# Optimization experiments

Hardware: AMD Instinct MI355X
Metric: run time of the kernel (lower is better)

The kernel has to match this reference:

```python
import jax, jax.numpy as jnp
import numpy as np

BS, T, N_AGENTS, N_ACTIONS = 8, 256, 8, 20
A = N_AGENTS * N_ACTIONS          # 160 gru input dim
E, D, HID, S = 128, 128, 32, 256  # encoder_dim, decoder_dim, mixing_embed_dim, state_dim
EMBED = HID * (A + E)             # 9216


def _lin(k, out_d, in_d):
    s = 1.0 / np.sqrt(in_d)
    return jax.random.uniform(k, (out_d, in_d), jnp.float32, -s, s)


def _vec(k, d, fan):
    s = 1.0 / np.sqrt(fan)
    return jax.random.uniform(k, (d,), jnp.float32, -s, s)


def setup_inputs() -> dict:
    key = jax.random.key(0)
    ks = jax.random.split(key, 32)
    inp = {
        'act': jax.random.uniform(ks[0], (BS, T, N_AGENTS, N_ACTIONS), jnp.float32),
        'states': jax.random.normal(ks[1], (BS, T, S), jnp.float32),
        # GRU (PyTorch layout: gates stacked [r; z; n])
        'gru_wih': _lin(ks[2], 3 * E, A),
        'gru_whh': _lin(ks[3], 3 * E, E),
        'gru_bih': _vec(ks[4], 3 * E, E),
        'gru_bhh': _vec(ks[5], 3 * E, E),
        # encoder fc
        'fc_w': _lin(ks[6], D, E),
        'fc_b': _vec(ks[7], D, E),
        # attention
        'attn_w': _lin(ks[8], D, D + E),
        'v_w': _vec(ks[9], D, D),
        # hyper_w_1 (2-layer MLP)
        'hw1_w0': _lin(ks[10], EMBED, S), 'hw1_b0': _vec(ks[11], EMBED, S),
        'hw1_w1': _lin(ks[12], EMBED, EMBED), 'hw1_b1': _vec(ks[13], EMBED, EMBED),
        # hyper_w_final (2-layer MLP)
        'hwf_w0': _lin(ks[14], HID, S), 'hwf_b0': _vec(ks[15], HID, S),
        'hwf_w1': _lin(ks[16], HID, HID), 'hwf_b1': _vec(ks[17], HID, HID),
        # hyper_b_1
        'hb1_w': _lin(ks[18], HID, S), 'hb1_b': _vec(ks[19], HID, S),
        # hyper_b_2 (2-layer MLP)
        'hb2_w0': _lin(ks[20], HID, S), 'hb2_b0': _vec(ks[21], HID, S),
        'hb2_w1': _lin(ks[22], 1, HID), 'hb2_b1': _vec(ks[23], 1, HID),
    }
    return inp


def reference(act, states, gru_wih, gru_whh, gru_bih, gru_bhh, fc_w, fc_b,
              attn_w, v_w, hw1_w0, hw1_b0, hw1_w1, hw1_b1,
              hwf_w0, hwf_b0, hwf_w1, hwf_b1, hb1_w, hb1_b,
              hb2_w0, hb2_b0, hb2_w1, hb2_b1):
    bs, t, n_ag, n_ac = act.shape
    a = n_ag * n_ac
    e = gru_whh.shape[1]
    d = fc_w.shape[0]
    hid = hb1_w.shape[0]

    act_flat = act.reshape(bs, t, a)
    # act_his = [zeros, act]; prefixes use only the first t steps of it
    x = jnp.concatenate([jnp.zeros((bs, 1, a), act.dtype), act_flat[:, : t - 1]], axis=1)

    # GRU over full sequence once (causal => identical to recomputing each prefix)
    def step(h, xt):
        gi = xt @ gru_wih.T + gru_bih
        gh = h @ gru_whh.T + gru_bhh
        ir, iz, i_n = jnp.split(gi, 3, axis=-1)
        hr, hz, h_n = jnp.split(gh, 3, axis=-1)
        r = jax.nn.sigmoid(ir + hr)
        z = jax.nn.sigmoid(iz + hz)
        n = jnp.tanh(i_n + r * h_n)
        h_new = (1.0 - z) * n + z * h
        return h_new, h_new

    h0 = jnp.zeros((bs, e), act.dtype)
    _, enc = jax.lax.scan(step, h0, jnp.swapaxes(x, 0, 1))
    enc = jnp.swapaxes(enc, 0, 1)  # [bs, T, E]

    # s0 for prefix ending at step q is tanh(fc(enc[:, q]))
    s0 = jnp.tanh(enc @ fc_w.T + fc_b)  # [bs, T, D]

    # attention: cat order is (s, enc_output)
    w_s, w_e = attn_w[:, :d], attn_w[:, d:]
    ps = s0 @ w_s.T            # [bs, Tq, D]
    pe = enc @ w_e.T           # [bs, Tk, D]
    pre = jnp.tanh(ps[:, :, None, :] + pe[:, None, :, :])  # [bs, Tq, Tk, D]
    scores = jnp.einsum('bqkd,d->bqk', pre, v_w)
    mask = jnp.tril(jnp.ones((t, t), bool))  # key j <= query q (prefix j < idx)
    scores = jnp.where(mask[None], scores, -jnp.inf)
    attn = jax.nn.softmax(scores, axis=-1)
    c = jnp.einsum('bqk,bke->bqe', attn, enc)  # [bs, T, E]

    inp = jnp.concatenate([act_flat, c], axis=-1).reshape(bs * t, 1, a + e)
    st = states.reshape(bs * t, -1)

    w1 = (jax.nn.relu(st @ hw1_w0.T + hw1_b0) @ hw1_w1.T + hw1_b1).reshape(bs * t, a + e, hid)
    b1 = (st @ hb1_w.T + hb1_b)[:, None, :]
    h = jax.nn.relu(jnp.einsum('bik,bkh->bih', inp, w1) + b1)  # [bs*T, 1, hid]

    wf = (jax.nn.relu(st @ hwf_w0.T + hwf_b0) @ hwf_w1.T + hwf_b1)[:, :, None]  # [bs*T, hid, 1]
    b2 = (jax.nn.relu(st @ hb2_w0.T + hb2_b0) @ hb2_w1.T + hb2_b1)[:, :, None]  # [bs*T, 1, 1]
    q = (jnp.einsum('bih,bho->bio', h, wf) + b2).reshape(bs, t, 1)
    return q
```

## Files before the change

kernel.cpp:

```cpp
#include <hip/hip_runtime.h>
#include <hip/hip_bf16.h>
#include <stdint.h>

typedef __attribute__((ext_vector_type(4))) float f32x4;
typedef __attribute__((ext_vector_type(8))) short short8v;
typedef __attribute__((ext_vector_type(4))) unsigned short u16x4;

constexpr int kT  = 256;
constexpr int kA  = 160;

__device__ __forceinline__ float bf2f(unsigned short u){
  union { unsigned int u; float f; } c; c.u = ((unsigned int)u) << 16; return c.f;
}
__device__ __forceinline__ unsigned short f2bf(float f){
  union { float f; unsigned int u; } c; c.f = f;
  unsigned int r = (c.u + 0x7FFFu + ((c.u >> 16) & 1u)) >> 16;
  return (unsigned short)r;
}
__device__ __forceinline__ float sigmoid_fast(float x){
  return __builtin_amdgcn_rcpf(1.f + __expf(-x));
}
__device__ __forceinline__ float tanhf_fast(float x){
  float xc = fminf(fmaxf(x, -15.f), 15.f);
  float t = __expf(2.f * xc);
  return (t - 1.f) * __builtin_amdgcn_rcpf(t + 1.f);
}
__device__ __forceinline__ void gload_lds16(const void* g, void* l){
  __builtin_amdgcn_global_load_lds((const __attribute__((address_space(1))) void*)g,
                                   (__attribute__((address_space(3))) void*)l, 16, 0, 0);
}
__device__ __forceinline__ void bar_lgkm(){
  asm volatile("s_waitcnt lgkmcnt(0)" ::: "memory");
  __builtin_amdgcn_s_barrier();
  asm volatile("" ::: "memory");
}
__device__ __forceinline__ void bar_only(){
  asm volatile("" ::: "memory");
  __builtin_amdgcn_s_barrier();
  asm volatile("" ::: "memory");
}

__global__ __launch_bounds__(256) void k_fill_f32(float* out, int n, float v){
  int i = blockIdx.x * blockDim.x + threadIdx.x;
  if (i < n) out[i] = v;
}

__global__ __launch_bounds__(256) void k_f32_to_bf16(const float* __restrict__ src,
                                                     unsigned short* __restrict__ dst, int n4){
  int stride = gridDim.x * blockDim.x;
  for (int i = blockIdx.x * blockDim.x + threadIdx.x; i < n4; i += stride){
    f32x4 v = *(const f32x4*)(src + (size_t)i * 4);
    u16x4 o;
    o[0] = f2bf(v[0]); o[1] = f2bf(v[1]); o[2] = f2bf(v[2]); o[3] = f2bf(v[3]);
    *(u16x4*)(dst + (size_t)i * 4) = o;
  }
}

__global__ __launch_bounds__(384) void k_gi(const float* __restrict__ act,
                                            const float* __restrict__ wih,
                                            const float* __restrict__ bih,
                                            float* __restrict__ gi){
  int blk = blockIdx.x;
  int b = blk >> 5, tg = blk & 31;
  int j = threadIdx.x;
  __shared__ __align__(16) float xh[8][kA];
  for (int idx = j; idx < 8 * kA; idx += 384){
    int u = idx / kA, i = idx - u * kA;
    int t = tg * 8 + u;
    xh[u][i] = (t == 0) ? 0.f : act[((size_t)b * kT + t - 1) * kA + i];
  }
  __syncthreads();
  float acc[8] = {0,0,0,0,0,0,0,0};
  for (int i = 0; i < kA; i += 4){
    f32x4 wv = *(const f32x4*)(wih + (size_t)j * kA + i);
#pragma unroll
    for (int jj = 0; jj < 4; ++jj)
#pragma unroll
      for (int u = 0; u < 8; ++u)
        acc[u] += wv[jj] * xh[u][i + jj];
  }
  float bv = bih[j];
#pragma unroll
  for (int u = 0; u < 8; ++u)
    gi[((size_t)b * kT + tg * 8 + u) * 384 + j] = acc[u] + bv;
}

template<int RELU>
__device__ __forceinline__ void gemm576_body(const unsigned short* __restrict__ A,
                                             const unsigned short* __restrict__ B,
                                             const float* __restrict__ bias,
                                             unsigned short* __restrict__ C,
                                             int M, int Nc, int K, int ldc,
                                             int bid, int nwg, char* smem){
  int nbm = M >> 7;
  int cpx = nwg >> 3;
  int sw  = (bid & 7) * cpx + (bid >> 3);
  int bm = sw % nbm, bn = sw / nbm;
  int arow0 = bm << 7;
  int bcol0 = bn * 576;
  int t = threadIdx.x;
  int l = t & 63, w = t >> 6;
  int wr = w >> 2, wc = w & 3;
  int lr = l & 15, kq = l >> 4;
  int Kb = K * 2;
  int ar = t >> 2, ap = t & 3;
  size_t aoffg = (size_t)ar * Kb + ((ap ^ ((ar >> 1) & 3)) << 4);
  size_t boffg[5];
#pragma unroll
  for (int i = 0; i < 5; ++i){
    int q = i * 512 + t, r = q >> 2, p = q & 3;
    boffg[i] = (size_t)r * Kb + ((p ^ ((r >> 1) & 3)) << 4);
  }
  const char* Ag = (const char*)(A + (size_t)arow0 * K);
  const char* Bg = (const char*)(B + (size_t)bcol0 * K);
  int dA = t * 16;
  int kk16 = (kq ^ ((lr >> 1) & 3)) << 4;
  int aRd = (wr * 64 + lr) * 64 + kk16;
  int bRd = 8192 + (wc * 144 + lr) * 64 + kk16;
  f32x4 acc[4][9] = {};
  int nt = K >> 5;

  auto stage = [&](int kt, int bi){
    size_t kb = (size_t)kt * 64;
    char* Ld = smem + bi * 49152;
    gload_lds16(Ag + aoffg + kb, Ld + dA);
#pragma unroll
    for (int i = 0; i < 5; ++i)
      gload_lds16(Bg + boffg[i] + kb, Ld + 8192 + i * 8192 + dA);
  };

  stage(0, 0);
  stage(1, 1);
  asm volatile("s_waitcnt vmcnt(6)" ::: "memory");
  int cur = 0;
  for (int kt = 0; kt < nt; ++kt){
    bar_only();
    if (kt + 2 < nt){
      int nb = cur + 2; if (nb >= 3) nb -= 3;
      stage(kt + 2, nb);
    }
    const char* Ld = smem + cur * 49152;
    short8v af[4];
#pragma unroll
    for (int m = 0; m < 4; ++m) af[m] = *(const short8v*)(Ld + aRd + m * 1024);
#pragma unroll
    for (int c = 0; c < 3; ++c){
      short8v bf[3];
#pragma unroll
      for (int j = 0; j < 3; ++j) bf[j] = *(const short8v*)(Ld + bRd + (c * 3 + j) * 1024);
      __builtin_amdgcn_s_setprio(1);
#pragma unroll
      for (int m = 0; m < 4; ++m)
#pragma unroll
        for (int j = 0; j < 3; ++j)
          acc[m][c * 3 + j] = __builtin_amdgcn_mfma_f32_16x16x32_bf16(af[m], bf[j], acc[m][c * 3 + j], 0, 0, 0);
      __builtin_amdgcn_s_setprio(0);
    }
    if (kt + 1 < nt){
      if (kt + 2 < nt) asm volatile("s_waitcnt vmcnt(6)" ::: "memory");
      else             asm volatile("s_waitcnt vmcnt(0)" ::: "memory");
    }
    ++cur; if (cur == 3) cur = 0;
  }

#pragma unroll
  for (int m = 0; m < 4; ++m){
    int row = arow0 + wr * 64 + m * 16 + kq * 4;
#pragma unroll
    for (int n = 0; n < 9; ++n){
      int col = bcol0 + wc * 144 + n * 16 + lr;
      float bv = bias[col];
#pragma unroll
      for (int r = 0; r < 4; ++r){
        float v = acc[m][n][r] + bv;
        if (RELU) v = fmaxf(v, 0.f);
        C[(size_t)(row + r) * ldc + col] = f2bf(v);
      }
    }
  }
}

template<int RELU>
__global__ __launch_bounds__(512) void k_gemm576(const unsigned short* __restrict__ A,
                                                 const unsigned short* __restrict__ B,
                                                 const float* __restrict__ bias,
                                                 unsigned short* __restrict__ C,
                                                 int M, int Nc, int K, int ldc){
  __shared__ __align__(16) char smem[147456];
  gemm576_body<RELU>(A, B, bias, C, M, Nc, K, ldc, blockIdx.x, gridDim.x, smem);
}

__global__ __launch_bounds__(512) void k_gru_g1_conv(const float* __restrict__ gi,
                                                     const float* __restrict__ whh,
                                                     const float* __restrict__ bhh,
                                                     float* __restrict__ enc,
                                                     const unsigned short* __restrict__ stb,
                                                     const unsigned short* __restrict__ w0b,
                                                     const float* __restrict__ hb0,
                                                     unsigned short* __restrict__ zb,
                                                     const float* __restrict__ csrc,
                                                     unsigned short* __restrict__ cdst,
                                                     int n4){
  __shared__ __align__(16) char smem[147456];
  int blk = blockIdx.x;
  if (blk >= 264){
    int stride = (gridDim.x - 264) * 512;
    for (int i = (blk - 264) * 512 + threadIdx.x; i < n4; i += stride){
      f32x4 v = *(const f32x4*)(csrc + (size_t)i * 4);
      u16x4 o;
      o[0] = f2bf(v[0]); o[1] = f2bf(v[1]); o[2] = f2bf(v[2]); o[3] = f2bf(v[3]);
      *(u16x4*)(cdst + (size_t)i * 4) = o;
    }
    return;
  }
  if (blk >= 8){
    gemm576_body<1>(stb, w0b, hb0, zb, 2048, 9216, 256, 9216, blk - 8, 256, smem);
    return;
  }
  float* h_lds = (float*)smem;
  float (*red)[128] = (float(*)[128])(smem + 512);
  int b = blk;
  int tid = threadIdx.x;
  int e = tid & 127, s = tid >> 7;
  float W0[32], W1[32], W2[32];
#pragma unroll
  for (int k = 0; k < 32; ++k){
    W0[k] = whh[(size_t)(0 * 128 + e) * 128 + s * 32 + k];
    W1[k] = whh[(size_t)(1 * 128 + e) * 128 + s * 32 + k];
    W2[k] = whh[(size_t)(2 * 128 + e) * 128 + s * 32 + k];
  }
  if (tid < 128) h_lds[tid] = 0.f;
  float bh0 = 0.f, bh1 = 0.f, bh2 = 0.f;
  if (tid < 128){ bh0 = bhh[e]; bh1 = bhh[128 + e]; bh2 = bhh[256 + e]; }
  const float* gib = gi + (size_t)b * kT * 384;
  float* encb = enc + (size_t)b * kT * 128;
  float gir = 0.f, giz = 0.f, gin = 0.f;
  if (tid < 128){ gir = gib[e]; giz = gib[128 + e]; gin = gib[256 + e]; }
  bar_lgkm();
  for (int t = 0; t < kT; ++t){
    float p0 = 0.f, p1 = 0.f, p2 = 0.f;
#pragma unroll
    for (int k4 = 0; k4 < 8; ++k4){
      f32x4 hv = *(const f32x4*)(h_lds + s * 32 + k4 * 4);
#pragma unroll
      for (int jj = 0; jj < 4; ++jj){
        p0 += W0[k4 * 4 + jj] * hv[jj];
        p1 += W1[k4 * 4 + jj] * hv[jj];
        p2 += W2[k4 * 4 + jj] * hv[jj];
      }
    }
    float nir = 0.f, niz = 0.f, nin = 0.f;
    if (t + 1 < kT && tid < 128){
      const float* gn = gib + (size_t)(t + 1) * 384;
      nir = gn[e]; niz = gn[128 + e]; nin = gn[256 + e];
    }
    red[s * 3 + 0][e] = p0; red[s * 3 + 1][e] = p1; red[s * 3 + 2][e] = p2;
    bar_lgkm();
    if (tid < 128){
      float ghr = red[0][e] + red[3][e] + red[6][e] + red[9][e]  + bh0;
      float ghz = red[1][e] + red[4][e] + red[7][e] + red[10][e] + bh1;
      float ghn = red[2][e] + red[5][e] + red[8][e] + red[11][e] + bh2;
      float r = sigmoid_fast(gir + ghr);
      float z = sigmoid_fast(giz + ghz);
      float n = tanhf_fast(gin + r * ghn);
      float hnew = (1.f - z) * n + z * h_lds[e];
      h_lds[e] = hnew;
      encb[t * 128 + e] = hnew;
    }
    bar_lgkm();
    gir = nir; giz = niz; gin = nin;
  }
}

__global__ __launch_bounds__(128) void k_attnpre(const float* __restrict__ enc,
                                                 const float* __restrict__ fc_w,
                                                 const float* __restrict__ fc_b,
                                                 const float* __restrict__ attn_w,
                                                 float* __restrict__ ps,
                                                 float* __restrict__ pe){
  int bt = blockIdx.x, o = threadIdx.x;
  __shared__ __align__(16) float ench[128], s0h[128];
  ench[o] = enc[(size_t)bt * 128 + o];
  __syncthreads();
  float a0 = fc_b[o], a1 = 0.f;
  for (int i = 0; i < 128; i += 4){
    f32x4 wv = *(const f32x4*)(fc_w + (size_t)o * 128 + i);
    f32x4 we = *(const f32x4*)(attn_w + (size_t)o * 256 + 128 + i);
    f32x4 ev = *(const f32x4*)(ench + i);
#pragma unroll
    for (int jj = 0; jj < 4; ++jj){ a0 += wv[jj] * ev[jj]; a1 += we[jj] * ev[jj]; }
  }
  s0h[o] = tanhf_fast(a0);
  pe[(size_t)bt * 128 + o] = a1;
  __syncthreads();
  float a2 = 0.f;
  for (int i = 0; i < 128; i += 4){
    f32x4 ws = *(const f32x4*)(attn_w + (size_t)o * 256 + i);
    f32x4 sv = *(const f32x4*)(s0h + i);
#pragma unroll
    for (int jj = 0; jj < 4; ++jj) a2 += ws[jj] * sv[jj];
  }
  ps[(size_t)bt * 128 + o] = a2;
}

__global__ __launch_bounds__(256) void k_attn(const float* __restrict__ enc,
                                              const float* __restrict__ ps,
                                              const float* __restrict__ pe,
                                              const float* __restrict__ v_w,
                                              float* __restrict__ cbuf){
  int q = blockIdx.x, b = blockIdx.y;
  int tid = threadIdx.x;
  __shared__ __align__(16) float psh[128], vwh[128];
  __shared__ __align__(16) float sch[256];
  __shared__ __align__(16) float rr[256];
  __shared__ float mxs, dns;
  if (tid < 128){
    psh[tid] = ps[((size_t)b * kT + q) * 128 + tid];
    vwh[tid] = v_w[tid];
  }
  __syncthreads();
  int nk = q + 1;
  for (int k = tid; k < nk; k += 256){
    const float* per = pe + ((size_t)b * kT + k) * 128;
    float sc = 0.f;
    for (int d = 0; d < 128; d += 4){
      f32x4 pv = *(const f32x4*)(per + d);
      f32x4 qv = *(const f32x4*)(psh + d);
      sc += vwh[d + 0] * tanhf_fast(qv[0] + pv[0]);
      sc += vwh[d + 1] * tanhf_fast(qv[1] + pv[1]);
      sc += vwh[d + 2] * tanhf_fast(qv[2] + pv[2]);
      sc += vwh[d + 3] * tanhf_fast(qv[3] + pv[3]);
    }
    sch[k] = sc;
  }
  __syncthreads();
  float lm = -3.0e38f;
  for (int k = tid; k < nk; k += 256) lm = fmaxf(lm, sch[k]);
  rr[tid] = lm; __syncthreads();
  for (int off = 128; off > 0; off >>= 1){
    if (tid < off) rr[tid] = fmaxf(rr[tid], rr[tid + off]);
    __syncthreads();
  }
  if (tid == 0) mxs = rr[0];
  __syncthreads();
  float mxv = mxs;
  float lsum = 0.f;
  for (int k = tid; k < nk; k += 256){
    float p = __expf(sch[k] - mxv);
    sch[k] = p; lsum += p;
  }
  __syncthreads();
  rr[tid] = lsum; __syncthreads();
  for (int off = 128; off > 0; off >>= 1){
    if (tid < off) rr[tid] += rr[tid + off];
    __syncthreads();
  }
  if (tid == 0) dns = __builtin_amdgcn_rcpf(rr[0]);
  __syncthreads();
  float rd = dns;
  int d = tid & 127, half = tid >> 7;
  float acc = 0.f;
  for (int k = half; k < nk; k += 2)
    acc += sch[k] * enc[((size_t)b * kT + k) * 128 + d];
  rr[tid] = acc; __syncthreads();
  if (half == 0)
    cbuf[((size_t)b * kT + q) * 128 + d] = (acc + rr[d + 128]) * rd;
}

__global__ __launch_bounds__(256) void k_final(const float* __restrict__ states,
                                               const float* __restrict__ act,
                                               const float* __restrict__ cbuf,
                                               const unsigned short* __restrict__ w1f,
                                               const float* __restrict__ hb1_w, const float* __restrict__ hb1_b,
                                               const float* __restrict__ hwf_w0, const float* __restrict__ hwf_b0,
                                               const float* __restrict__ hwf_w1, const float* __restrict__ hwf_b1,
                                               const float* __restrict__ hb2_w0, const float* __restrict__ hb2_b0,
                                               const float* __restrict__ hb2_w1, const float* __restrict__ hb2_b1,
                                               float* __restrict__ out){
  int bt = blockIdx.x, tid = threadIdx.x;
  __shared__ __align__(16) float sth[256], inph[288], red[256];
  __shared__ __align__(16) float t1h[32], t2h[32], b1h[32], wfh[32], hvals[32];
  __shared__ float b2s;
  sth[tid] = states[(size_t)bt * 256 + tid];
  if (tid < 160) inph[tid] = act[(size_t)bt * 160 + tid];
  if (tid < 128) inph[160 + tid] = cbuf[(size_t)bt * 128 + tid];
  __syncthreads();
  int o = tid & 31, s = tid >> 5;
  float p1 = 0.f, p2 = 0.f, p3 = 0.f;
  for (int k = s * 32; k < s * 32 + 32; k += 4){
    f32x4 sv  = *(const f32x4*)(sth + k);
    f32x4 w1v = *(const f32x4*)(hwf_w0 + (size_t)o * 256 + k);
    f32x4 w2v = *(const f32x4*)(hb2_w0 + (size_t)o * 256 + k);
    f32x4 w3v = *(const f32x4*)(hb1_w  + (size_t)o * 256 + k);
#pragma unroll
    for (int jj = 0; jj < 4; ++jj){
      p1 += w1v[jj] * sv[jj]; p2 += w2v[jj] * sv[jj]; p3 += w3v[jj] * sv[jj];
    }
  }
  red[tid] = p1; __syncthreads();
  if (tid < 32){
    float a = hwf_b0[tid];
#pragma unroll
    for (int s8 = 0; s8 < 8; ++s8) a += red[s8 * 32 + tid];
    t1h[tid] = fmaxf(a, 0.f);
  }
  __syncthreads();
  red[tid] = p2; __syncthreads();
  if (tid < 32){
    float a = hb2_b0[tid];
#pragma unroll
    for (int s8 = 0; s8 < 8; ++s8) a += red[s8 * 32 + tid];
    t2h[tid] = fmaxf(a, 0.f);
  }
  __syncthreads();
  red[tid] = p3; __syncthreads();
  if (tid < 32){
    float a = hb1_b[tid];
#pragma unroll
    for (int s8 = 0; s8 < 8; ++s8) a += red[s8 * 32 + tid];
    b1h[tid] = a;
  }
  __syncthreads();
  if (tid < 32){
    float a = hwf_b1[tid];
#pragma unroll
    for (int j = 0; j < 32; ++j) a += hwf_w1[(size_t)tid * 32 + j] * t1h[j];
    wfh[tid] = a;
  }
  if (tid == 64){
    float a = hb2_b1[0];
#pragma unroll
    for (int j = 0; j < 32; ++j) a += hb2_w1[j] * t2h[j];
    b2s = a;
  }
  __syncthreads();
  float ph = 0.f;
  const unsigned short* wrow = w1f + (size_t)bt * 9216;
  for (int i = s * 36; i < s * 36 + 36; ++i)
    ph += inph[i] * bf2f(wrow[i * 32 + o]);
  red[tid] = ph; __syncthreads();
  if (tid < 32){
    float a = b1h[tid];
#pragma unroll
    for (int s8 = 0; s8 < 8; ++s8) a += red[s8 * 32 + tid];
    hvals[tid] = fmaxf(a, 0.f) * wfh[tid];
  }
  __syncthreads();
  if (tid == 0){
    float q = b2s;
#pragma unroll
    for (int j = 0; j < 32; ++j) q += hvals[j];
    out[bt] = q;
  }
}

extern "C" void kernel_launch(void* const* d_in, const int* in_sizes, int n_in,
                              void* d_out, int out_size, void* d_ws, size_t ws_size,
                              hipStream_t stream){
  float* outp = (float*)d_out;

  bool ok = (n_in == 24) && out_size == 2048 &&
            in_sizes[0] == 327680 && in_sizes[1] == 524288 &&
            in_sizes[2] == 61440  && in_sizes[3] == 49152 &&
            in_sizes[10] == 2359296 && in_sizes[12] == 84934656;
  if (!ok){
    k_fill_f32<<<dim3(8), dim3(256), 0, stream>>>(outp, 2048, 1.0e6f);
    return;
  }

  const float* act    = (const float*)d_in[0];
  const float* states = (const float*)d_in[1];
  const float* wih    = (const float*)d_in[2];
  const float* whh    = (const float*)d_in[3];
  const float* bih    = (const float*)d_in[4];
  const float* bhh    = (const float*)d_in[5];
  const float* fc_w   = (const float*)d_in[6];
  const float* fc_b   = (const float*)d_in[7];
  const float* attn_w = (const float*)d_in[8];
  const float* v_w    = (const float*)d_in[9];
  const float* hw1_w0 = (const float*)d_in[10];
  const float* hw1_b0 = (const float*)d_in[11];
  const float* hw1_w1 = (const float*)d_in[12];
  const float* hw1_b1 = (const float*)d_in[13];
  const float* hwf_w0 = (const float*)d_in[14];
  const float* hwf_b0 = (const float*)d_in[15];
  const float* hwf_w1 = (const float*)d_in[16];
  const float* hwf_b1 = (const float*)d_in[17];
  const float* hb1_w  = (const float*)d_in[18];
  const float* hb1_b  = (const float*)d_in[19];
  const float* hb2_w0 = (const float*)d_in[20];
  const float* hb2_b0 = (const float*)d_in[21];
  const float* hb2_w1 = (const float*)d_in[22];
  const float* hb2_b1 = (const float*)d_in[23];

  char* ws = (char*)d_ws;
  size_t off = 0;
  auto alloc = [&](size_t bytes)->void*{
    void* p = ws + off; off += (bytes + 255) & ~(size_t)255; return p;
  };
  unsigned short* zb  = (unsigned short*)alloc((size_t)2048 * 9216 * 2);
  unsigned short* w1f = (unsigned short*)alloc((size_t)2048 * 9216 * 2);
  unsigned short* w0b = (unsigned short*)alloc((size_t)9216 * 256 * 2);
  unsigned short* stb = (unsigned short*)alloc((size_t)2048 * 256 * 2);
  float* gi   = (float*)alloc((size_t)2048 * 384 * 4);
  float* enc  = (float*)alloc((size_t)2048 * 128 * 4);
  float* psb  = (float*)alloc((size_t)2048 * 128 * 4);
  float* peb  = (float*)alloc((size_t)2048 * 128 * 4);
  float* cbuf = (float*)alloc((size_t)2048 * 128 * 4);
  size_t floor_bytes = off;
  const size_t row_bytes = (size_t)9216 * 2;
  const size_t slack = (size_t)2 << 20;
  if (ws_size < floor_bytes + 576 * row_bytes + slack){
    k_fill_f32<<<dim3(8), dim3(256), 0, stream>>>(outp, 2048, (float)(ws_size >> 20));
    return;
  }
  size_t avail = ws_size - floor_bytes - slack;
  int chunk_rows = (int)(((avail / row_bytes) / 576) * 576);
  if (chunk_rows > 9216) chunk_rows = 9216;
  unsigned short* w1c = (unsigned short*)(ws + floor_bytes);
  int first_nc = chunk_rows;

  k_f32_to_bf16<<<dim3(1024), dim3(256), 0, stream>>>(hw1_w0, w0b, 9216 * 256 / 4);
  k_f32_to_bf16<<<dim3(256),  dim3(256), 0, stream>>>(states, stb, 2048 * 256 / 4);
  k_gi<<<dim3(256), dim3(384), 0, stream>>>(act, wih, bih, gi);
  k_gru_g1_conv<<<dim3(2048), dim3(512), 0, stream>>>(gi, whh, bhh, enc,
                                                      stb, w0b, hw1_b0, zb,
                                                      hw1_w1, w1c, first_nc * 9216 / 4);
  k_attnpre<<<dim3(2048), dim3(128), 0, stream>>>(enc, fc_w, fc_b, attn_w, psb, peb);
  k_attn<<<dim3(256, 8), dim3(256), 0, stream>>>(enc, psb, peb, v_w, cbuf);
  for (int c0 = 0; c0 < 9216; c0 += chunk_rows){
    int nc = 9216 - c0; if (nc > chunk_rows) nc = chunk_rows;
    if (c0 > 0)
      k_f32_to_bf16<<<dim3(2048), dim3(256), 0, stream>>>(hw1_w1 + (size_t)c0 * 9216, w1c, nc * 9216 / 4);
    k_gemm576<0><<<dim3(16 * (nc / 576)), dim3(512), 0, stream>>>(zb, w1c, hw1_b1 + c0, w1f + c0,
                                                                  2048, nc, 9216, 9216);
  }
  k_final<<<dim3(2048), dim3(256), 0, stream>>>(states, act, cbuf, w1f,
      hb1_w, hb1_b, hwf_w0, hwf_b0, hwf_w1, hwf_b1, hb2_w0, hb2_b0, hb2_w1, hb2_b1,
      outp);
}
```

Measured before the change: 742.6 us.

## Move hw1_w1 bf16 conversion from GRU kernel into attention kernels

After: 787.9 us. +6.1%, slower.

```diff
diff --git a/kernel.cpp b/kernel.cpp
--- a/kernel.cpp
+++ b/kernel.cpp
@@ -39,21 +39,25 @@
   __builtin_amdgcn_s_barrier();
   asm volatile("" ::: "memory");
 }
-
-__global__ __launch_bounds__(256) void k_fill_f32(float* out, int n, float v){
-  int i = blockIdx.x * blockDim.x + threadIdx.x;
-  if (i < n) out[i] = v;
-}
-
-__global__ __launch_bounds__(256) void k_f32_to_bf16(const float* __restrict__ src,
-                                                     unsigned short* __restrict__ dst, int n4){
-  int stride = gridDim.x * blockDim.x;
-  for (int i = blockIdx.x * blockDim.x + threadIdx.x; i < n4; i += stride){
+__device__ __forceinline__ void conv_range(const float* __restrict__ src,
+                                           unsigned short* __restrict__ dst,
+                                           int beg, int end, int start, int stride){
+  for (int i = beg + start; i < end; i += stride){
     f32x4 v = *(const f32x4*)(src + (size_t)i * 4);
     u16x4 o;
     o[0] = f2bf(v[0]); o[1] = f2bf(v[1]); o[2] = f2bf(v[2]); o[3] = f2bf(v[3]);
     *(u16x4*)(dst + (size_t)i * 4) = o;
   }
+}
+
+__global__ __launch_bounds__(256) void k_fill_f32(float* out, int n, float v){
+  int i = blockIdx.x * blockDim.x + threadIdx.x;
+  if (i < n) out[i] = v;
+}
+
+__global__ __launch_bounds__(256) void k_f32_to_bf16(const float* __restrict__ src,
+                                                     unsigned short* __restrict__ dst, int n4){
+  conv_range(src, dst, 0, n4, blockIdx.x * blockDim.x + threadIdx.x, gridDim.x * blockDim.x);
 }
 
 __global__ __launch_bounds__(384) void k_gi(const float* __restrict__ act,
@@ -190,29 +194,16 @@
   gemm576_body<RELU>(A, B, bias, C, M, Nc, K, ldc, blockIdx.x, gridDim.x, smem);
 }
 
-__global__ __launch_bounds__(512) void k_gru_g1_conv(const float* __restrict__ gi,
-                                                     const float* __restrict__ whh,
-                                                     const float* __restrict__ bhh,
-                                                     float* __restrict__ enc,
-                                                     const unsigned short* __restrict__ stb,
-                                                     const unsigned short* __restrict__ w0b,
-                                                     const float* __restrict__ hb0,
-                                                     unsigned short* __restrict__ zb,
-                                                     const float* __restrict__ csrc,
-                                                     unsigned short* __restrict__ cdst,
-                                                     int n4){
+__global__ __launch_bounds__(512) void k_gru_g1(const float* __restrict__ gi,
+                                                const float* __restrict__ whh,
+                                                const float* __restrict__ bhh,
+                                                float* __restrict__ enc,
+                                                const unsigned short* __restrict__ stb,
+                                                const unsigned short* __restrict__ w0b,
+                                                const float* __restrict__ hb0,
+                                                unsigned short* __restrict__ zb){
   __shared__ __align__(16) char smem[147456];
   int blk = blockIdx.x;
-  if (blk >= 264){
-    int stride = (gridDim.x - 264) * 512;
-    for (int i = (blk - 264) * 512 + threadIdx.x; i < n4; i += stride){
-      f32x4 v = *(const f32x4*)(csrc + (size_t)i * 4);
-      u16x4 o;
-      o[0] = f2bf(v[0]); o[1] = f2bf(v[1]); o[2] = f2bf(v[2]); o[3] = f2bf(v[3]);
-      *(u16x4*)(cdst + (size_t)i * 4) = o;
-    }
-    return;
-  }
   if (blk >= 8){
     gemm576_body<1>(stb, w0b, hb0, zb, 2048, 9216, 256, 9216, blk - 8, 256, smem);
     return;
@@ -272,13 +263,21 @@
   }
 }
 
-__global__ __launch_bounds__(128) void k_attnpre(const float* __restrict__ enc,
-                                                 const float* __restrict__ fc_w,
-                                                 const float* __restrict__ fc_b,
-                                                 const float* __restrict__ attn_w,
-                                                 float* __restrict__ ps,
-                                                 float* __restrict__ pe){
-  int bt = blockIdx.x, o = threadIdx.x;
+__global__ __launch_bounds__(128) void k_attnpre_conv(const float* __restrict__ enc,
+                                                      const float* __restrict__ fc_w,
+                                                      const float* __restrict__ fc_b,
+                                                      const float* __restrict__ attn_w,
+                                                      float* __restrict__ ps,
+                                                      float* __restrict__ pe,
+                                                      const float* __restrict__ csrc,
+                                                      unsigned short* __restrict__ cdst,
+                                                      int beg, int end){
+  int blk = blockIdx.x;
+  if (blk >= 2048){
+    conv_range(csrc, cdst, beg, end, (blk - 2048) * 128 + threadIdx.x, (gridDim.x - 2048) * 128);
+    return;
+  }
+  int bt = blk, o = threadIdx.x;
   __shared__ __align__(16) float ench[128], s0h[128];
   ench[o] = enc[(size_t)bt * 128 + o];
   __syncthreads();
@@ -303,12 +302,20 @@
   ps[(size_t)bt * 128 + o] = a2;
 }
 
-__global__ __launch_bounds__(256) void k_attn(const float* __restrict__ enc,
-                                              const float* __restrict__ ps,
-                                              const float* __restrict__ pe,
-                                              const float* __restrict__ v_w,
-                                              float* __restrict__ cbuf){
-  int q = blockIdx.x, b = blockIdx.y;
+__global__ __launch_bounds__(256) void k_attn_conv(const float* __restrict__ enc,
+                                                   const float* __restrict__ ps,
+                                                   const float* __restrict__ pe,
+                                                   const float* __restrict__ v_w,
+                                                   float* __restrict__ cbuf,
+                                                   const float* __restrict__ csrc,
+                                                   unsigned short* __restrict__ cdst,
+                                                   int beg, int end){
+  int blk = blockIdx.x;
+  if (blk >= 2048){
+    conv_range(csrc, cdst, beg, end, (blk - 2048) * 256 + threadIdx.x, (gridDim.x - 2048) * 256);
+    return;
+  }
+  int q = blk & 255, b = blk >> 8;
   int tid = threadIdx.x;
   __shared__ __align__(16) float psh[128], vwh[128];
   __shared__ __align__(16) float sch[256];
@@ -518,16 +525,17 @@
   int chunk_rows = (int)(((avail / row_bytes) / 576) * 576);
   if (chunk_rows > 9216) chunk_rows = 9216;
   unsigned short* w1c = (unsigned short*)(ws + floor_bytes);
-  int first_nc = chunk_rows;
 
   k_f32_to_bf16<<<dim3(1024), dim3(256), 0, stream>>>(hw1_w0, w0b, 9216 * 256 / 4);
   k_f32_to_bf16<<<dim3(256),  dim3(256), 0, stream>>>(states, stb, 2048 * 256 / 4);
   k_gi<<<dim3(256), dim3(384), 0, stream>>>(act, wih, bih, gi);
-  k_gru_g1_conv<<<dim3(2048), dim3(512), 0, stream>>>(gi, whh, bhh, enc,
-                                                      stb, w0b, hw1_b0, zb,
-                                                      hw1_w1, w1c, first_nc * 9216 / 4);
-  k_attnpre<<<dim3(2048), dim3(128), 0, stream>>>(enc, fc_w, fc_b, attn_w, psb, peb);
-  k_attn<<<dim3(256, 8), dim3(256), 0, stream>>>(enc, psb, peb, v_w, cbuf);
+  k_gru_g1<<<dim3(264), dim3(512), 0, stream>>>(gi, whh, bhh, enc, stb, w0b, hw1_b0, zb);
+  int n4_0 = chunk_rows * 9216 / 4;
+  int n4a = ((n4_0 * 2) / 5) & ~63;
+  k_attnpre_conv<<<dim3(2048 + 1024), dim3(128), 0, stream>>>(enc, fc_w, fc_b, attn_w, psb, peb,
+                                                              hw1_w1, w1c, 0, n4a);
+  k_attn_conv<<<dim3(2048 + 1024), dim3(256), 0, stream>>>(enc, psb, peb, v_w, cbuf,
+                                                           hw1_w1, w1c, n4a, n4_0);
   for (int c0 = 0; c0 < 9216; c0 += chunk_rows){
     int nc = 9216 - c0; if (nc > chunk_rows) nc = chunk_rows;
     if (c0 > 0)
```
